# Kernel optimization log

Hardware: AMD Instinct MI355X
Metric: run time of the kernel (lower is better)

## Reference

```python
import jax, jax.numpy as jnp
import numpy as np

N = 50000      # nodes
E = 1600000    # edges per graph
IN = 64
HID = 64
OUT = 64


def _gat_conv(x, edge_index, W, a_src, a_dst, bias):
    """PyG GATConv, heads=1, add_self_loops=True, negative_slope=0.2."""
    n = x.shape[0]
    h = x @ W                                   # [N, d]
    loop = jnp.arange(n, dtype=edge_index.dtype)
    src = jnp.concatenate([edge_index[0], loop])
    dst = jnp.concatenate([edge_index[1], loop])
    e = jax.nn.leaky_relu((h @ a_src)[src] + (h @ a_dst)[dst], negative_slope=0.2)
    m = jax.ops.segment_max(e, dst, num_segments=n)          # stable edge-softmax per dst
    w = jnp.exp(e - m[dst])
    denom = jax.ops.segment_sum(w, dst, num_segments=n)
    alpha = w / denom[dst]                                   # [E+N]
    out = jax.ops.segment_sum(h[src] * alpha[:, None], dst, num_segments=n)
    return out + bias


def setup_inputs() -> dict:
    key = jax.random.key(0)
    ks = jax.random.split(key, 32)

    def glorot(k, shape):
        fan_out = shape[1] if len(shape) > 1 else 1
        lim = (6.0 / (shape[0] + fan_out)) ** 0.5
        return jax.random.uniform(k, shape, minval=-lim, maxval=lim, dtype=jnp.float32)

    inp = {
        "x_ind": jax.random.normal(ks[0], (N, IN), jnp.float32),
        "x_pos": jax.random.normal(ks[1], (N, IN), jnp.float32),
        "edge_ind": jax.random.randint(ks[2], (2, E), 0, N, dtype=jnp.int32),
        "edge_pos": jax.random.randint(ks[3], (2, E), 0, N, dtype=jnp.int32),
        "w1_ind": glorot(ks[4], (IN, HID)),
        "as1_ind": glorot(ks[5], (HID,)),
        "ad1_ind": glorot(ks[6], (HID,)),
        "b1_ind": jnp.zeros((HID,), jnp.float32),
        "w2_ind": glorot(ks[7], (HID, OUT)),
        "as2_ind": glorot(ks[8], (OUT,)),
        "ad2_ind": glorot(ks[9], (OUT,)),
        "b2_ind": jnp.zeros((OUT,), jnp.float32),
        "w1_pos": glorot(ks[10], (IN, HID)),
        "as1_pos": glorot(ks[11], (HID,)),
        "ad1_pos": glorot(ks[12], (HID,)),
        "b1_pos": jnp.zeros((HID,), jnp.float32),
        "w2_pos": glorot(ks[13], (HID, OUT)),
        "as2_pos": glorot(ks[14], (OUT,)),
        "ad2_pos": glorot(ks[15], (OUT,)),
        "b2_pos": jnp.zeros((OUT,), jnp.float32),
        "first_hop_att": glorot(ks[16], (2, HID)),
        "att_weight": glorot(ks[17], (2, OUT)),
        "mlp_w": glorot(ks[18], (OUT, 1)),
        "mlp_b": jnp.zeros((1,), jnp.float32),
    }
    return inp


def reference(x_ind, x_pos, edge_ind, edge_pos,
              w1_ind, as1_ind, ad1_ind, b1_ind,
              w2_ind, as2_ind, ad2_ind, b2_ind,
              w1_pos, as1_pos, ad1_pos, b1_pos,
              w2_pos, as2_pos, ad2_pos, b2_pos,
              first_hop_att, att_weight, mlp_w, mlp_b):
    h_i = jax.nn.relu(_gat_conv(x_ind, edge_ind, w1_ind, as1_ind, ad1_ind, b1_ind))
    h_p = jax.nn.relu(_gat_conv(x_pos, edge_pos, w1_pos, as1_pos, ad1_pos, b1_pos))
    # first-hop branch attention over the two graphs
    s1 = jnp.stack([jnp.sum(first_hop_att[0] * h_i, axis=1),
                    jnp.sum(first_hop_att[1] * h_p, axis=1)], axis=0)  # [2, N]
    a1 = jax.nn.softmax(s1, axis=0)
    fused = a1[0][:, None] * h_i + a1[1][:, None] * h_p
    g_i = _gat_conv(fused, edge_ind, w2_ind, as2_ind, ad2_ind, b2_ind)
    g_p = _gat_conv(fused, edge_pos, w2_pos, as2_pos, ad2_pos, b2_pos)
    s2 = jnp.stack([jnp.sum(att_weight[0] * g_i, axis=1),
                    jnp.sum(att_weight[1] * g_p, axis=1)], axis=0)
    a2 = jax.nn.softmax(s2, axis=0)
    x = a2[0][:, None] * g_i + a2[1][:, None] * g_p
    return x @ mlp_w + mlp_b                    # [N, 1]
```

## Files before the change

### kernel.cpp

```cpp
#include <hip/hip_runtime.h>
#include <hip/hip_fp16.h>

#define ND 64
#define BG 256
#define MAXB 512
#define PCH 16384
#define CAP 9216

__device__ __forceinline__ float lrelu(float x) { return x > 0.f ? x : 0.2f * x; }

__device__ __forceinline__ float wave_sum(float v) {
#pragma unroll
    for (int m = 32; m > 0; m >>= 1) v += __shfl_xor(v, m, 64);
    return v;
}

__device__ __forceinline__ void fma8(float* acc, float w, int4 raw) {
    union { int4 i; __half2 h[4]; } u;
    u.i = raw;
#pragma unroll
    for (int i = 0; i < 4; i++) {
        float2 f = __half22float2(u.h[i]);
        acc[2 * i]     = fmaf(w, f.x, acc[2 * i]);
        acc[2 * i + 1] = fmaf(w, f.y, acc[2 * i + 1]);
    }
}


__global__ void init_cursor(int* __restrict__ bcursor, int nb) {
    int t = threadIdx.x;
    if (t < nb) bcursor[t] = t * CAP;
}

__device__ void partition_body(int* hist, int* lcur,
                               const int* __restrict__ eI, const int* __restrict__ eP,
                               int* __restrict__ bcursor, int* __restrict__ part,
                               int N, int E, int nb) {
    int t = threadIdx.x;
    int total = 2 * E;
    int chunkBase = blockIdx.x * PCH;
    int cnt = min(PCH, total - chunkBase);
    int cnt4 = cnt & ~3;
    if (t < nb) hist[t] = 0;
    __syncthreads();
    for (int i = t * 4; i < cnt4; i += 4096) {
        int e = chunkBase + i;
        int4 d; int base;
        if (e + 3 < E)   { d = *(const int4*)(eI + E + e); base = 0; }
        else if (e >= E) { d = *(const int4*)(eP + E + (e - E)); base = N; }
        else {
            int tmp[4];
#pragma unroll
            for (int k = 0; k < 4; k++) {
                int ee = e + k;
                tmp[k] = (ee < E) ? eI[E + ee] : N + eP[E + ee - E];
            }
            d = make_int4(tmp[0], tmp[1], tmp[2], tmp[3]); base = 0;
        }
        atomicAdd(&hist[(base + d.x) >> 8], 1);
        atomicAdd(&hist[(base + d.y) >> 8], 1);
        atomicAdd(&hist[(base + d.z) >> 8], 1);
        atomicAdd(&hist[(base + d.w) >> 8], 1);
    }
    for (int i = cnt4 + t; i < cnt; i += 1024) {
        int e = chunkBase + i;
        int idx = (e < E) ? eI[E + e] : N + eP[E + (e - E)];
        atomicAdd(&hist[idx >> 8], 1);
    }
    __syncthreads();
    if (t < nb) lcur[t] = hist[t] ? atomicAdd(&bcursor[t], hist[t]) : 0;
    __syncthreads();
    for (int i = t * 4; i < cnt4; i += 4096) {
        int e = chunkBase + i;
        int4 s4, d4; int base;
        if (e + 3 < E)   { s4 = *(const int4*)(eI + e); d4 = *(const int4*)(eI + E + e); base = 0; }
        else if (e >= E) { s4 = *(const int4*)(eP + (e - E)); d4 = *(const int4*)(eP + E + (e - E)); base = N; }
        else {
            int ts[4], td[4];
#pragma unroll
            for (int k = 0; k < 4; k++) {
                int ee = e + k;
                if (ee < E) { ts[k] = eI[ee]; td[k] = eI[E + ee]; }
                else        { ts[k] = eP[ee - E]; td[k] = N + eP[E + ee - E]; }
            }
            s4 = make_int4(ts[0], ts[1], ts[2], ts[3]);
            d4 = make_int4(td[0], td[1], td[2], td[3]); base = 0;
        }
        int idx, pos;
        idx = base + d4.x; pos = atomicAdd(&lcur[idx >> 8], 1); part[pos] = (s4.x << 8) | (idx & 255);
        idx = base + d4.y; pos = atomicAdd(&lcur[idx >> 8], 1); part[pos] = (s4.y << 8) | (idx & 255);
        idx = base + d4.z; pos = atomicAdd(&lcur[idx >> 8], 1); part[pos] = (s4.z << 8) | (idx & 255);
        idx = base + d4.w; pos = atomicAdd(&lcur[idx >> 8], 1); part[pos] = (s4.w << 8) | (idx & 255);
    }
    for (int i = cnt4 + t; i < cnt; i += 1024) {
        int e = chunkBase + i;
        int s, idx;
        if (e < E) { s = eI[e]; idx = eI[E + e]; }
        else       { s = eP[e - E]; idx = N + eP[E + (e - E)]; }
        int pos = atomicAdd(&lcur[idx >> 8], 1);
        part[pos] = (s << 8) | (idx & 255);
    }
}

__device__ void gemm_body(float* xsAll, int gb,
                          const float* __restrict__ xA, const float* __restrict__ xB,
                          const float* __restrict__ WA, const float* __restrict__ WB,
                          const float* __restrict__ asA, const float* __restrict__ adA,
                          const float* __restrict__ asB, const float* __restrict__ adB,
                          __half* __restrict__ h16, float* __restrict__ ssrc,
                          float* __restrict__ sdst, int N) {
    int half = gb & 1;
    int blk = gb >> 1;
    int wave = threadIdx.x >> 6;
    int lane = threadIdx.x & 63;
    const float* x  = half ? xB : xA;
    const float* W  = half ? WB : WA;
    const float* av_ = half ? asB : asA;
    const float* dv_ = half ? adB : adA;
    int nodeBase = (blk * 16 + wave) * 4;
    float* xs = xsAll + wave * (4 * ND);

    if (nodeBase + 3 < N) {
        *(float4*)&xs[lane * 4] = *(const float4*)&x[(size_t)nodeBase * ND + lane * 4];
    } else if (nodeBase < N) {
#pragma unroll
        for (int i = 0; i < 4; i++) {
            int gi = nodeBase * ND + lane * 4 + i;
            xs[lane * 4 + i] = (gi < N * ND) ? x[gi] : 0.f;
        }
    }
    __syncthreads();
    if (nodeBase >= N) return;

    float4 acc = {0.f, 0.f, 0.f, 0.f};
#pragma unroll
    for (int k = 0; k < ND; k++) {
        float wv = W[k * ND + lane];
        acc.x = fmaf(xs[0 * ND + k], wv, acc.x);
        acc.y = fmaf(xs[1 * ND + k], wv, acc.y);
        acc.z = fmaf(xs[2 * ND + k], wv, acc.z);
        acc.w = fmaf(xs[3 * ND + k], wv, acc.w);
    }
    float av = av_[lane], dv = dv_[lane];
    float s1x = wave_sum(acc.x * av), s2x = wave_sum(acc.x * dv);
    float s1y = wave_sum(acc.y * av), s2y = wave_sum(acc.y * dv);
    float s1z = wave_sum(acc.z * av), s2z = wave_sum(acc.z * dv);
    float s1w = wave_sum(acc.w * av), s2w = wave_sum(acc.w * dv);

    int g0 = half * N + nodeBase;
    h16[(size_t)(g0 + 0) * ND + lane] = __float2half(acc.x);
    if (nodeBase + 1 < N) h16[(size_t)(g0 + 1) * ND + lane] = __float2half(acc.y);
    if (nodeBase + 2 < N) h16[(size_t)(g0 + 2) * ND + lane] = __float2half(acc.z);
    if (nodeBase + 3 < N) h16[(size_t)(g0 + 3) * ND + lane] = __float2half(acc.w);
    if (lane == 0) {
        ssrc[g0] = s1x; sdst[g0] = s2x;
        if (nodeBase + 1 < N) { ssrc[g0 + 1] = s1y; sdst[g0 + 1] = s2y; }
        if (nodeBase + 2 < N) { ssrc[g0 + 2] = s1z; sdst[g0 + 2] = s2z; }
        if (nodeBase + 3 < N) { ssrc[g0 + 3] = s1w; sdst[g0 + 3] = s2w; }
    }
}

__global__ void __launch_bounds__(1024) part_gemm(
        const int* __restrict__ eI, const int* __restrict__ eP,
        int* __restrict__ bcursor, int* __restrict__ part,
        const float* __restrict__ xA, const float* __restrict__ xB,
        const float* __restrict__ WA, const float* __restrict__ WB,
        const float* __restrict__ asA, const float* __restrict__ adA,
        const float* __restrict__ asB, const float* __restrict__ adB,
        __half* __restrict__ h16, float* __restrict__ ssrc, float* __restrict__ sdst,
        int N, int E, int nb, int partBlocks) {
    __shared__ int smem[16 * 4 * ND];
    if (blockIdx.x < partBlocks) {
        partition_body(smem, smem + MAXB, eI, eP, bcursor, part, N, E, nb);
    } else {
        gemm_body((float*)smem, blockIdx.x - partBlocks,
                  xA, xB, WA, WB, asA, adA, asB, adB, h16, ssrc, sdst, N);
    }
}

__global__ void bucket_build(const int* __restrict__ part, const int* __restrict__ bcursor,
                             int* __restrict__ row, int* __restrict__ deg,
                             int* __restrict__ csr, int n2, int N) {
    __shared__ int lhist[BG * 4];
    __shared__ int lrow[BG * 4];
    int b = blockIdx.x, t = threadIdx.x;
    int start = b * CAP;
    int cnt = bcursor[b] - start;
    int cnt4 = cnt & ~3;
    int q1 = N >> 2, q2 = N >> 1, q3 = q1 + q2;
    auto key = [&](int p) {
        int s = p >> 8;
        int q = (s >= q2) ? 2 : 0;
        q += (s >= (q ? q3 : q1)) ? 1 : 0;
        return ((p & 255) << 2) | q;
    };
    lhist[t] = 0;
    __syncthreads();
    for (int j = t * 4; j < cnt4; j += 4096) {
        int4 p = *(const int4*)(part + start + j);
        atomicAdd(&lhist[key(p.x)], 1);
        atomicAdd(&lhist[key(p.y)], 1);
        atomicAdd(&lhist[key(p.z)], 1);
        atomicAdd(&lhist[key(p.w)], 1);
    }
    for (int j = cnt4 + t; j < cnt; j += 1024) atomicAdd(&lhist[key(part[start + j])], 1);
    __syncthreads();
    int v = lhist[t];
    lrow[t] = v;
    __syncthreads();
    for (int off = 1; off < 1024; off <<= 1) {
        int a = (t >= off) ? lrow[t - off] : 0;
        __syncthreads();
        lrow[t] += a;
        __syncthreads();
    }
    int cur = start + lrow[t] - v;
    if (t < BG) {
        int g = b * BG + t;
        if (g < n2) {
            row[g] = start + lrow[4 * t] - lhist[4 * t];
            deg[g] = lhist[4 * t] + lhist[4 * t + 1] + lhist[4 * t + 2] + lhist[4 * t + 3];
        }
    }
    __syncthreads();
    lhist[t] = cur;
    __syncthreads();
    for (int j = t * 4; j < cnt4; j += 4096) {
        int4 p = *(const int4*)(part + start + j);
        int pos;
        pos = atomicAdd(&lhist[key(p.x)], 1); csr[pos] = p.x >> 8;
        pos = atomicAdd(&lhist[key(p.y)], 1); csr[pos] = p.y >> 8;
        pos = atomicAdd(&lhist[key(p.z)], 1); csr[pos] = p.z >> 8;
        pos = atomicAdd(&lhist[key(p.w)], 1); csr[pos] = p.w >> 8;
    }
    for (int j = cnt4 + t; j < cnt; j += 1024) {
        int p = part[start + j];
        int pos = atomicAdd(&lhist[key(p)], 1);
        csr[pos] = p >> 8;
    }
}

__global__ void gemm2_fused(const float* __restrict__ hbig, const float* __restrict__ fha,
                            const float* __restrict__ WA, const float* __restrict__ WB,
                            const float* __restrict__ asA, const float* __restrict__ adA,
                            const float* __restrict__ asB, const float* __restrict__ adB,
                            __half* __restrict__ h16, float* __restrict__ ssrc,
                            float* __restrict__ sdst, int N) {
    __shared__ float xs[4][4 * ND];
    int half = blockIdx.x & 1;
    int blk = blockIdx.x >> 1;
    int wave = threadIdx.x >> 6;
    int lane = threadIdx.x & 63;
    const float* W  = half ? WB : WA;
    const float* av_ = half ? asB : asA;
    const float* dv_ = half ? adB : adA;
    int nodeBase = (blk * 4 + wave) * 4;
    float* xsw = xs[wave];

    if (nodeBase < N) {
        int nd = nodeBase + (lane >> 4);
        int col = (lane & 15) * 4;
        float4 vi = *(const float4*)&hbig[(size_t)nd * ND + col];
        float4 vp = *(const float4*)&hbig[((size_t)N + nd) * ND + col];
        float4 a0 = *(const float4*)&fha[col];
        float4 a1 = *(const float4*)&fha[ND + col];
        float p0 = vi.x * a0.x + vi.y * a0.y + vi.z * a0.z + vi.w * a0.w;
        float p1 = vp.x * a1.x + vp.y * a1.y + vp.z * a1.z + vp.w * a1.w;
#pragma unroll
        for (int m = 1; m <= 8; m <<= 1) {
            p0 += __shfl_xor(p0, m, 64);
            p1 += __shfl_xor(p1, m, 64);
        }
        float mx = fmaxf(p0, p1);
        float e0 = __expf(p0 - mx), e1 = __expf(p1 - mx);
        float inv = 1.f / (e0 + e1);
        float4 f;
        f.x = (e0 * vi.x + e1 * vp.x) * inv;
        f.y = (e0 * vi.y + e1 * vp.y) * inv;
        f.z = (e0 * vi.z + e1 * vp.z) * inv;
        f.w = (e0 * vi.w + e1 * vp.w) * inv;
        *(float4*)&xsw[lane * 4] = f;
    }
    __syncthreads();
    if (nodeBase >= N) return;

    float4 acc = {0.f, 0.f, 0.f, 0.f};
#pragma unroll
    for (int k = 0; k < ND; k++) {
        float wv = W[k * ND + lane];
        acc.x = fmaf(xsw[0 * ND + k], wv, acc.x);
        acc.y = fmaf(xsw[1 * ND + k], wv, acc.y);
        acc.z = fmaf(xsw[2 * ND + k], wv, acc.z);
        acc.w = fmaf(xsw[3 * ND + k], wv, acc.w);
    }
    float av = av_[lane], dv = dv_[lane];
    float s1x = wave_sum(acc.x * av), s2x = wave_sum(acc.x * dv);
    float s1y = wave_sum(acc.y * av), s2y = wave_sum(acc.y * dv);
    float s1z = wave_sum(acc.z * av), s2z = wave_sum(acc.z * dv);
    float s1w = wave_sum(acc.w * av), s2w = wave_sum(acc.w * dv);

    int g0 = half * N + nodeBase;
    h16[(size_t)(g0 + 0) * ND + lane] = __float2half(acc.x);
    h16[(size_t)(g0 + 1) * ND + lane] = __float2half(acc.y);
    h16[(size_t)(g0 + 2) * ND + lane] = __float2half(acc.z);
    h16[(size_t)(g0 + 3) * ND + lane] = __float2half(acc.w);
    if (lane == 0) {
        ssrc[g0] = s1x; sdst[g0] = s2x;
        ssrc[g0 + 1] = s1y; sdst[g0 + 1] = s2y;
        ssrc[g0 + 2] = s1z; sdst[g0 + 2] = s2z;
        ssrc[g0 + 3] = s1w; sdst[g0 + 3] = s2w;
    }
}

__global__ void aggregate_dual(const int* __restrict__ csr, const int* __restrict__ row,
                               const int* __restrict__ deg, const float* __restrict__ ssrc,
                               const float* __restrict__ sdst, const __half* __restrict__ h16,
                               const float* __restrict__ bA, const float* __restrict__ bB,
                               float* __restrict__ out, int N, int relu) {
    int half = blockIdx.x & 1;
    int wave = threadIdx.x >> 6;
    int lane = threadIdx.x & 63;
    int sub  = lane >> 4;
    int l16  = lane & 15;
    int slot = l16 >> 3;
    int fl8  = (l16 & 7) * 8;
    int node = ((blockIdx.x >> 1) * 4 + wave) * 4 + sub;
    bool valid = node < N;
    int g = half * N + node;
    const float* bias = half ? bB : bA;
    const float* ss = ssrc + (size_t)half * N;
    const __half* hh = h16 + (size_t)half * N * ND;

    int start = valid ? row[g] : 0;
    int cnt   = valid ? deg[g] : 0;
    float sd  = valid ? sdst[g] : 0.f;
    float wself = valid ? __expf(lrelu(ss[node] + sd)) : 0.f;

    float acc[8] = {0.f, 0.f, 0.f, 0.f, 0.f, 0.f, 0.f, 0.f};
    float denomp = 0.f;
    int waveBase = sub << 4;

    for (int base = 0; base < cnt; base += 16) {
        int c16 = min(16, cnt - base);
        int sj = (l16 < c16) ? csr[start + base + l16] : 0;
        float wj = (l16 < c16) ? __expf(lrelu(ss[sj] + sd)) : 0.f;
        denomp += wj;
        int nq = (c16 + 1) >> 1;
        float w0 = __shfl(wj, waveBase + slot, 64);
        int s0 = __shfl(sj, waveBase + slot, 64);
        int4 r0 = *(const int4*)(hh + (size_t)s0 * ND + fl8);
        if (nq == 1) { fma8(acc, w0, r0); continue; }
        float w1 = __shfl(wj, waveBase + 2 + slot, 64);
        int s1 = __shfl(sj, waveBase + 2 + slot, 64);
        int4 r1 = *(const int4*)(hh + (size_t)s1 * ND + fl8);
        for (int c = 2; c < nq; c++) {
            float w2 = __shfl(wj, waveBase + c * 2 + slot, 64);
            int s2 = __shfl(sj, waveBase + c * 2 + slot, 64);
            int4 r2 = *(const int4*)(hh + (size_t)s2 * ND + fl8);
            fma8(acc, w0, r0);
            w0 = w1; r0 = r1;
            w1 = w2; r1 = r2;
        }
        fma8(acc, w0, r0);
        fma8(acc, w1, r1);
    }

#pragma unroll
    for (int i = 0; i < 8; i++) acc[i] += __shfl_xor(acc[i], 8, 64);
#pragma unroll
    for (int m = 1; m <= 8; m <<= 1) denomp += __shfl_xor(denomp, m, 64);
    float denom = denomp + wself;

    if (!valid || slot != 0) return;
    int4 rawS = *(const int4*)(hh + (size_t)node * ND + fl8);
    union { int4 i; __half2 h[4]; } us;
    us.i = rawS;
    float v[8];
#pragma unroll
    for (int i = 0; i < 4; i++) {
        float2 f = __half22float2(us.h[i]);
        v[2 * i]     = (acc[2 * i]     + wself * f.x) / denom + bias[fl8 + 2 * i];
        v[2 * i + 1] = (acc[2 * i + 1] + wself * f.y) / denom + bias[fl8 + 2 * i + 1];
    }
    if (relu) {
#pragma unroll
        for (int i = 0; i < 8; i++) v[i] = fmaxf(v[i], 0.f);
    }
    *(float4*)&out[(size_t)g * ND + fl8]     = make_float4(v[0], v[1], v[2], v[3]);
    *(float4*)&out[(size_t)g * ND + fl8 + 4] = make_float4(v[4], v[5], v[6], v[7]);
}

__global__ void branch_att_mlp(const float* __restrict__ hbig, const float* __restrict__ att,
                               const float* __restrict__ mlpw, const float* __restrict__ mlpb,
                               float* __restrict__ out, int n) {
    int gid = blockIdx.x * blockDim.x + threadIdx.x;
    int node = gid >> 6, lane = gid & 63;
    if (node >= n) return;
    float vi = hbig[(size_t)node * ND + lane];
    float vp = hbig[((size_t)n + node) * ND + lane];
    float s0 = wave_sum(att[lane] * vi);
    float s1 = wave_sum(att[ND + lane] * vp);
    float m = fmaxf(s0, s1);
    float a0 = __expf(s0 - m), a1 = __expf(s1 - m);
    float xj = (a0 * vi + a1 * vp) / (a0 + a1);
    float o = wave_sum(xj * mlpw[lane]);
    if (lane == 0) out[node] = o + mlpb[0];
}

extern "C" void kernel_launch(void* const* d_in, const int* in_sizes, int n_in,
                              void* d_out, int out_size, void* d_ws, size_t ws_size,
                              hipStream_t stream) {
    const int N = in_sizes[0] / ND;
    const int E = in_sizes[2] / 2;

    const float* x_ind = (const float*)d_in[0];
    const float* x_pos = (const float*)d_in[1];
    const int*   e_ind = (const int*)d_in[2];
    const int*   e_pos = (const int*)d_in[3];
    const float* w1i = (const float*)d_in[4];
    const float* as1i = (const float*)d_in[5];
    const float* ad1i = (const float*)d_in[6];
    const float* b1i = (const float*)d_in[7];
    const float* w2i = (const float*)d_in[8];
    const float* as2i = (const float*)d_in[9];
    const float* ad2i = (const float*)d_in[10];
    const float* b2i = (const float*)d_in[11];
    const float* w1p = (const float*)d_in[12];
    const float* as1p = (const float*)d_in[13];
    const float* ad1p = (const float*)d_in[14];
    const float* b1p = (const float*)d_in[15];
    const float* w2p = (const float*)d_in[16];
    const float* as2p = (const float*)d_in[17];
    const float* ad2p = (const float*)d_in[18];
    const float* b2p = (const float*)d_in[19];
    const float* fha = (const float*)d_in[20];
    const float* attw = (const float*)d_in[21];
    const float* mlpw = (const float*)d_in[22];
    const float* mlpb = (const float*)d_in[23];

    char* ws = (char*)d_ws;
    size_t off = 0;
    auto alloc = [&](size_t elems) { void* p = ws + off; off += elems * 4; return p; };

    const int n2 = 2 * N;
    const int nb = (n2 + BG - 1) / BG;

    __half* h16 = (__half*)alloc((size_t)n2 * ND / 2);
    float* hbig = (float*)alloc((size_t)n2 * ND);
    float* ssrc = (float*)alloc(n2);
    float* sdst = (float*)alloc(n2);
    int* deg    = (int*)alloc(n2);
    int* rowi   = (int*)alloc(n2);
    int* csr    = (int*)alloc((size_t)nb * CAP);
    int* bcursor= (int*)alloc(MAXB);
    int* part   = (int*)hbig;

    const int partBlocks  = (2 * E + PCH - 1) / PCH;
    const int gemm1Blocks = 2 * ((N + 63) / 64);
    const int gemm2Blocks = 2 * ((N + 15) / 16);
    const int aggBlocks   = 2 * ((N + 15) / 16);
    const int nodeBlocks  = (N + 3) / 4;

    init_cursor<<<1, 512, 0, stream>>>(bcursor, nb);
    part_gemm<<<partBlocks + gemm1Blocks, 1024, 0, stream>>>(
        e_ind, e_pos, bcursor, part,
        x_ind, x_pos, w1i, w1p, as1i, ad1i, as1p, ad1p,
        h16, ssrc, sdst, N, E, nb, partBlocks);
    bucket_build<<<nb, 1024, 0, stream>>>(part, bcursor, rowi, deg, csr, n2, N);

    aggregate_dual<<<aggBlocks, 256, 0, stream>>>(csr, rowi, deg, ssrc, sdst, h16,
                                                  b1i, b1p, hbig, N, 1);

    gemm2_fused<<<gemm2Blocks, 256, 0, stream>>>(hbig, fha, w2i, w2p,
                                                 as2i, ad2i, as2p, ad2p,
                                                 h16, ssrc, sdst, N);
    aggregate_dual<<<aggBlocks, 256, 0, stream>>>(csr, rowi, deg, ssrc, sdst, h16,
                                                  b2i, b2p, hbig, N, 0);
    branch_att_mlp<<<nodeBlocks, 256, 0, stream>>>(hbig, attw, mlpw, mlpb,
                                                   (float*)d_out, N);
}
```

Before: 331.8 us.

## Single-pass register-cached edge partition and prefetch next neighbor chunk in aggregation

For full chunks, the partition kernel now loads each edge once into registers, packing payloads and bucket ids while building the histogram, then scatters from registers instead of re-reading the edge arrays. The aggregation loop prefetches the next 16 CSR indices and their source scores before processing the current batch, hiding gather latency. The half-to-float conversion is rewritten element-wise. This raises register pressure in both kernels, which may lower occupancy.

Result: no change. 328.9 us (-0.9%).

```diff
diff --git a/kernel.cpp b/kernel.cpp
--- a/kernel.cpp
+++ b/kernel.cpp
@@ -16,14 +16,10 @@
 }
 
 __device__ __forceinline__ void fma8(float* acc, float w, int4 raw) {
-    union { int4 i; __half2 h[4]; } u;
+    union { int4 i; __half h[8]; } u;
     u.i = raw;
 #pragma unroll
-    for (int i = 0; i < 4; i++) {
-        float2 f = __half22float2(u.h[i]);
-        acc[2 * i]     = fmaf(w, f.x, acc[2 * i]);
-        acc[2 * i + 1] = fmaf(w, f.y, acc[2 * i + 1]);
-    }
+    for (int i = 0; i < 8; i++) acc[i] = fmaf(w, __half2float(u.h[i]), acc[i]);
 }
 
 
@@ -40,9 +36,58 @@
     int total = 2 * E;
     int chunkBase = blockIdx.x * PCH;
     int cnt = min(PCH, total - chunkBase);
+    if (t < nb) hist[t] = 0;
+    __syncthreads();
+
+    if (cnt == PCH) {
+        int pk[16];
+        unsigned bkp[8];
+#pragma unroll
+        for (int it = 0; it < 4; it++) {
+            int i = t * 4 + it * 4096;
+            int e = chunkBase + i;
+            int sv[4], dv[4];
+            if (e + 3 < E) {
+                int4 a = *(const int4*)(eI + e);
+                int4 b = *(const int4*)(eI + E + e);
+                sv[0] = a.x; sv[1] = a.y; sv[2] = a.z; sv[3] = a.w;
+                dv[0] = b.x; dv[1] = b.y; dv[2] = b.z; dv[3] = b.w;
+            } else if (e >= E) {
+                int4 a = *(const int4*)(eP + (e - E));
+                int4 b = *(const int4*)(eP + E + (e - E));
+                sv[0] = a.x; sv[1] = a.y; sv[2] = a.z; sv[3] = a.w;
+                dv[0] = b.x + N; dv[1] = b.y + N; dv[2] = b.z + N; dv[3] = b.w + N;
+            } else {
+#pragma unroll
+                for (int k = 0; k < 4; k++) {
+                    int ee = e + k;
+                    if (ee < E) { sv[k] = eI[ee]; dv[k] = eI[E + ee]; }
+                    else        { sv[k] = eP[ee - E]; dv[k] = N + eP[E + ee - E]; }
+                }
+            }
+#pragma unroll
+            for (int k = 0; k < 4; k++) {
+                int j = it * 4 + k;
+                int bk = dv[k] >> 8;
+                pk[j] = (sv[k] << 8) | (dv[k] & 255);
+                atomicAdd(&hist[bk], 1);
+                if ((j & 1) == 0) bkp[j >> 1] = (unsigned)bk;
+                else bkp[j >> 1] |= (unsigned)bk << 16;
+            }
+        }
+        __syncthreads();
+        if (t < nb) lcur[t] = hist[t] ? atomicAdd(&bcursor[t], hist[t]) : 0;
+        __syncthreads();
+#pragma unroll
+        for (int j = 0; j < 16; j++) {
+            int bk = (bkp[j >> 1] >> ((j & 1) * 16)) & 0xffff;
+            int pos = atomicAdd(&lcur[bk], 1);
+            part[pos] = pk[j];
+        }
+        return;
+    }
+
     int cnt4 = cnt & ~3;
-    if (t < nb) hist[t] = 0;
-    __syncthreads();
     for (int i = t * 4; i < cnt4; i += 4096) {
         int e = chunkBase + i;
         int4 d; int base;
@@ -70,29 +115,7 @@
     __syncthreads();
     if (t < nb) lcur[t] = hist[t] ? atomicAdd(&bcursor[t], hist[t]) : 0;
     __syncthreads();
-    for (int i = t * 4; i < cnt4; i += 4096) {
-        int e = chunkBase + i;
-        int4 s4, d4; int base;
-        if (e + 3 < E)   { s4 = *(const int4*)(eI + e); d4 = *(const int4*)(eI + E + e); base = 0; }
-        else if (e >= E) { s4 = *(const int4*)(eP + (e - E)); d4 = *(const int4*)(eP + E + (e - E)); base = N; }
-        else {
-            int ts[4], td[4];
-#pragma unroll
-            for (int k = 0; k < 4; k++) {
-                int ee = e + k;
-                if (ee < E) { ts[k] = eI[ee]; td[k] = eI[E + ee]; }
-                else        { ts[k] = eP[ee - E]; td[k] = N + eP[E + ee - E]; }
-            }
-            s4 = make_int4(ts[0], ts[1], ts[2], ts[3]);
-            d4 = make_int4(td[0], td[1], td[2], td[3]); base = 0;
-        }
-        int idx, pos;
-        idx = base + d4.x; pos = atomicAdd(&lcur[idx >> 8], 1); part[pos] = (s4.x << 8) | (idx & 255);
-        idx = base + d4.y; pos = atomicAdd(&lcur[idx >> 8], 1); part[pos] = (s4.y << 8) | (idx & 255);
-        idx = base + d4.z; pos = atomicAdd(&lcur[idx >> 8], 1); part[pos] = (s4.z << 8) | (idx & 255);
-        idx = base + d4.w; pos = atomicAdd(&lcur[idx >> 8], 1); part[pos] = (s4.w << 8) | (idx & 255);
-    }
-    for (int i = cnt4 + t; i < cnt; i += 1024) {
+    for (int i = t; i < cnt; i += 1024) {
         int e = chunkBase + i;
         int s, idx;
         if (e < E) { s = eI[e]; idx = eI[E + e]; }
@@ -340,29 +363,43 @@
     float denomp = 0.f;
     int waveBase = sub << 4;
 
+    int c16 = min(16, cnt);
+    int sj = (l16 < c16) ? csr[start + l16] : 0;
+    float wj = (l16 < c16) ? __expf(lrelu(ss[sj] + sd)) : 0.f;
+
     for (int base = 0; base < cnt; base += 16) {
-        int c16 = min(16, cnt - base);
-        int sj = (l16 < c16) ? csr[start + base + l16] : 0;
-        float wj = (l16 < c16) ? __expf(lrelu(ss[sj] + sd)) : 0.f;
+        int nb2 = base + 16;
+        int sjn = 0; float svn = 0.f; int c16n = cnt - nb2;
+        if (nb2 < cnt) {
+            sjn = (l16 < c16n) ? csr[start + nb2 + l16] : 0;
+            svn = (l16 < c16n) ? ss[sjn] : 0.f;
+        }
         denomp += wj;
-        int nq = (c16 + 1) >> 1;
+        int nq = (min(16, cnt - base) + 1) >> 1;
         float w0 = __shfl(wj, waveBase + slot, 64);
         int s0 = __shfl(sj, waveBase + slot, 64);
         int4 r0 = *(const int4*)(hh + (size_t)s0 * ND + fl8);
-        if (nq == 1) { fma8(acc, w0, r0); continue; }
-        float w1 = __shfl(wj, waveBase + 2 + slot, 64);
-        int s1 = __shfl(sj, waveBase + 2 + slot, 64);
-        int4 r1 = *(const int4*)(hh + (size_t)s1 * ND + fl8);
-        for (int c = 2; c < nq; c++) {
-            float w2 = __shfl(wj, waveBase + c * 2 + slot, 64);
-            int s2 = __shfl(sj, waveBase + c * 2 + slot, 64);
-            int4 r2 = *(const int4*)(hh + (size_t)s2 * ND + fl8);
+        if (nq > 1) {
+            float w1 = __shfl(wj, waveBase + 2 + slot, 64);
+            int s1 = __shfl(sj, waveBase + 2 + slot, 64);
+            int4 r1 = *(const int4*)(hh + (size_t)s1 * ND + fl8);
+            for (int c = 2; c < nq; c++) {
+                float w2 = __shfl(wj, waveBase + c * 2 + slot, 64);
+                int s2 = __shfl(sj, waveBase + c * 2 + slot, 64);
+                int4 r2 = *(const int4*)(hh + (size_t)s2 * ND + fl8);
+                fma8(acc, w0, r0);
+                w0 = w1; r0 = r1;
+                w1 = w2; r1 = r2;
+            }
             fma8(acc, w0, r0);
-            w0 = w1; r0 = r1;
-            w1 = w2; r1 = r2;
-        }
-        fma8(acc, w0, r0);
-        fma8(acc, w1, r1);
+            fma8(acc, w1, r1);
+        } else {
+            fma8(acc, w0, r0);
+        }
+        if (nb2 < cnt) {
+            wj = (l16 < c16n) ? __expf(lrelu(svn + sd)) : 0.f;
+            sj = sjn;
+        }
     }
 
 #pragma unroll
@@ -373,15 +410,12 @@
 
     if (!valid || slot != 0) return;
     int4 rawS = *(const int4*)(hh + (size_t)node * ND + fl8);
-    union { int4 i; __half2 h[4]; } us;
+    union { int4 i; __half h[8]; } us;
     us.i = rawS;
     float v[8];
 #pragma unroll
-    for (int i = 0; i < 4; i++) {
-        float2 f = __half22float2(us.h[i]);
-        v[2 * i]     = (acc[2 * i]     + wself * f.x) / denom + bias[fl8 + 2 * i];
-        v[2 * i + 1] = (acc[2 * i + 1] + wself * f.y) / denom + bias[fl8 + 2 * i + 1];
-    }
+    for (int i = 0; i < 8; i++)
+        v[i] = (acc[i] + wself * __half2float(us.h[i])) / denom + bias[fl8 + i];
     if (relu) {
 #pragma unroll
         for (int i = 0; i < 8; i++) v[i] = fmaxf(v[i], 0.f);
```
